# Optimization experiments

Hardware: AMD Instinct MI355X
Metric: run time of the kernel (lower is better)

The kernel has to match this reference:

```python
import jax, jax.numpy as jnp
import numpy as np

EMBED_DIM = 128
N_HEADS = 8
HEAD_DEPTH = EMBED_DIM // N_HEADS  # 16
CLIP = 10.0
B, N = 256, 1000


def setup_inputs() -> dict:
    key = jax.random.key(0)
    ks = jax.random.split(key, 10)
    D = EMBED_DIM
    return {
        "node_embeddings": jax.random.normal(ks[0], (B, N, D), jnp.float32),
        "graph_embedding": jax.random.normal(ks[1], (B, D), jnp.float32),
        "step_context": jax.random.normal(ks[2], (B, 1, D + 2), jnp.float32),
        "mask": jax.random.randint(ks[3], (B, 1, N), 0, 2).astype(bool),
        "Wk1": jax.random.normal(ks[4], (D, D), jnp.float32) / np.sqrt(D),
        "Wv": jax.random.normal(ks[5], (D, D), jnp.float32) / np.sqrt(D),
        "Wk2": jax.random.normal(ks[6], (D, D), jnp.float32) / np.sqrt(D),
        "Wq_fixed": jax.random.normal(ks[7], (D, D), jnp.float32) / np.sqrt(D),
        "Wout": jax.random.normal(ks[8], (D, D), jnp.float32) / np.sqrt(D),
        "Wq_step": jax.random.normal(ks[9], (D + 2, D), jnp.float32) / np.sqrt(D),
    }


def reference(node_embeddings, graph_embedding, step_context, mask,
              Wk1, Wv, Wk2, Wq_fixed, Wout, Wq_step):
    b, n, D = node_embeddings.shape
    H, dh = N_HEADS, HEAD_DEPTH
    neg_inf = jnp.float32(-1e9)

    # compute_static: precomputed projections of node/graph embeddings
    K1 = node_embeddings @ Wk1                      # [B,N,D]
    V = node_embeddings @ Wv                        # [B,N,D]
    K2 = node_embeddings @ Wk2                      # [B,N,D]
    Q_fixed = graph_embedding[:, None, :] @ Wq_fixed  # [B,1,D]

    # compute_dynamic: single-query masked MHA
    Q_step = step_context @ Wq_step                 # [B,1,D]
    Q1 = Q_fixed + Q_step                           # [B,1,D]
    q = Q1.reshape(b, 1, H, dh)
    k = K1.reshape(b, n, H, dh)
    v = V.reshape(b, n, H, dh)
    score = jnp.einsum('bqhd,bkhd->bhqk', q, k) / jnp.sqrt(jnp.float32(dh))
    score = jnp.where(mask[:, None, :, :], neg_inf, score)  # mask [B,1,N] -> [B,1,1,N]
    attn = jax.nn.softmax(score, axis=-1)           # [B,H,1,N]
    mha = jnp.einsum('bhqk,bkhd->bqhd', attn, v).reshape(b, 1, D)
    Q2 = mha @ Wout                                 # [B,1,D]

    # SHA: clipped single-head logits over all nodes
    logits = CLIP * jnp.tanh(
        jnp.einsum('bqd,bkd->bqk', Q2, K2) / jnp.sqrt(jnp.float32(D)))  # [B,1,N]
    logits = jnp.where(mask, neg_inf, logits)
    return logits[:, 0, :]                          # [B,N]
```

## Files before the change

### kernel.cpp

```cpp
#include <hip/hip_runtime.h>
#include <stdint.h>


#define DD 128
#define NH 8
#define DHD 16
#define NS 8
#define TILE 64
#define RP 132
#define SP 9
#define NMAX_PAD 1024

typedef short v8s __attribute__((ext_vector_type(8)));
typedef float v4f __attribute__((ext_vector_type(4)));

__device__ __forceinline__ unsigned short f2bf(float x) {
    unsigned u = __float_as_uint(x);
    u += 0x7fffu + ((u >> 16) & 1u);
    return (unsigned short)(u >> 16);
}

__device__ __forceinline__ bool detect_mask32(const void* maskp) {
    const uint32_t* mw = (const uint32_t*)maskp;
    bool m32 = true;
    #pragma unroll
    for (int i = 0; i < 16; ++i) m32 = m32 && (mw[i] <= 1u);
    return m32;
}

__global__ __launch_bounds__(128)
void k0_prep(const float* __restrict__ graph, const float* __restrict__ ctx,
             const float* __restrict__ Wk1, const float* __restrict__ Wqf,
             const float* __restrict__ Wqs, float* __restrict__ wq_ws)
{
    __shared__ float q1[DD];
    const int b = blockIdx.x, tid = threadIdx.x;
    const float* ge = graph + (size_t)b * DD;
    const float* sc = ctx + (size_t)b * (DD + 2);
    float acc = 0.f;
    #pragma unroll 4
    for (int k = 0; k < DD; ++k)     acc += ge[k] * Wqf[k * DD + tid];
    #pragma unroll 4
    for (int k = 0; k < DD + 2; ++k) acc += sc[k] * Wqs[k * DD + tid];
    q1[tid] = acc;
    __syncthreads();
    const float* wrow = Wk1 + (size_t)tid * DD;
    #pragma unroll
    for (int h = 0; h < NH; ++h) {
        float a = 0.f;
        #pragma unroll
        for (int j = 0; j < DHD; ++j) a += wrow[h * DHD + j] * q1[h * DHD + j];
        wq_ws[(size_t)b * NH * DD + h * DD + tid] = 0.25f * a;
    }
}

__global__ __launch_bounds__(512)
void kA_mfma(const float* __restrict__ node, const float* __restrict__ wq_ws,
             const void* __restrict__ maskp, float* __restrict__ spart_ws,
             float* __restrict__ mz_ws, int N)
{
    __shared__ __align__(16) unsigned short tA[2][8][64][16];
    __shared__ __align__(16) unsigned short Ph[2][16][72];
    __shared__ float wmax[16][9];
    __shared__ float zpart[16][9];
    __shared__ float mfin[16];

    const int b = blockIdx.y, j = blockIdx.x, tid = threadIdx.x;
    const int lane = tid & 63, w = tid >> 6;
    const int c = lane & 15, g = lane >> 4;
    const int rows = (N + NS - 1) / NS;
    const int n0 = j * rows;
    const int nend = min(n0 + rows, N);

    if (nend <= n0) {
        float* sp = spart_ws + ((size_t)b * NS + j) * NH * DD;
        for (int o = tid; o < NH * DD; o += 512) sp[o] = 0.f;
        if (tid < NH) {
            float* mzp = mz_ws + (((size_t)b * NS + j) * NH + tid) * 2;
            mzp[0] = -1e30f; mzp[1] = 0.f;
        }
        return;
    }

    const bool m32 = detect_mask32(maskp);
    const int32_t* mi = (const int32_t*)maskp + (size_t)b * N;
    const uint8_t* mb = (const uint8_t*)maskp + (size_t)b * N;
    const float* nodeB = node + (size_t)b * N * DD;

    v8s aw[4];
    #pragma unroll
    for (int kk = 0; kk < 4; ++kk) {
        v8s a;
        #pragma unroll
        for (int i = 0; i < 8; ++i) a[i] = 0;
        if (c < NH) {
            const float* wr = wq_ws + (size_t)b * NH * DD + (size_t)c * DD + kk * 32 + g * 8;
            #pragma unroll
            for (int i = 0; i < 8; ++i) a[i] = (short)f2bf(wr[i]);
        }
        aw[kk] = a;
    }

    {
        const int L = tid >> 3, c8 = tid & 7;
        #pragma unroll
        for (int t = 0; t < 2; ++t) {
            const int n = n0 + t * 64 + L;
            unsigned short tmp[16];
            if (n < nend) {
                const float4* src = (const float4*)(nodeB + (size_t)n * DD + c8 * 16);
                #pragma unroll
                for (int k = 0; k < 4; ++k) {
                    const float4 v = src[k];
                    tmp[4*k+0] = f2bf(v.x); tmp[4*k+1] = f2bf(v.y);
                    tmp[4*k+2] = f2bf(v.z); tmp[4*k+3] = f2bf(v.w);
                }
            } else {
                #pragma unroll
                for (int k = 0; k < 16; ++k) tmp[k] = 0;
            }
            *(v8s*)&tA[t][c8][L][0] = *(v8s*)&tmp[0];
            *(v8s*)&tA[t][c8][L][8] = *(v8s*)&tmp[8];
        }
    }
    __syncthreads();

    const int ts = w >> 2, rg = w & 3;
    const int nrow = n0 + ts * 64 + rg * 16 + c;
    v4f sc = {0.f, 0.f, 0.f, 0.f};
    #pragma unroll
    for (int kk = 0; kk < 4; ++kk) {
        const v8s bfrag = *(const v8s*)&tA[ts][kk * 2 + (g >> 1)][rg * 16 + c][(g & 1) * 8];
        sc = __builtin_amdgcn_mfma_f32_16x16x32_bf16(aw[kk], bfrag, sc, 0, 0, 0);
    }

    float s4[4];
    {
        const bool valid = nrow < nend;
        const bool msk = valid && (m32 ? (mi[nrow] != 0) : (mb[nrow] != 0));
        #pragma unroll
        for (int r = 0; r < 4; ++r)
            s4[r] = !valid ? -1e30f : (msk ? -1e9f : sc[r]);
    }

    {
        float mx[4];
        #pragma unroll
        for (int r = 0; r < 4; ++r) mx[r] = s4[r];
        #pragma unroll
        for (int d = 1; d < 16; d <<= 1) {
            #pragma unroll
            for (int r = 0; r < 4; ++r) mx[r] = fmaxf(mx[r], __shfl_xor(mx[r], d));
        }
        if (c == 0) {
            #pragma unroll
            for (int r = 0; r < 4; ++r) wmax[g * 4 + r][w] = mx[r];
        }
    }
    __syncthreads();
    if (w == 0 && lane < 16) {
        float m = wmax[lane][0];
        #pragma unroll
        for (int ww = 1; ww < 8; ++ww) m = fmaxf(m, wmax[lane][ww]);
        mfin[lane] = m;
    }
    __syncthreads();

    {
        float e4[4];
        #pragma unroll
        for (int r = 0; r < 4; ++r) e4[r] = __expf(s4[r] - mfin[g * 4 + r]);
        float zr[4];
        #pragma unroll
        for (int r = 0; r < 4; ++r) zr[r] = e4[r];
        #pragma unroll
        for (int d = 1; d < 16; d <<= 1) {
            #pragma unroll
            for (int r = 0; r < 4; ++r) zr[r] += __shfl_xor(zr[r], d);
        }
        if (c == 0) {
            #pragma unroll
            for (int r = 0; r < 4; ++r) zpart[g * 4 + r][w] = zr[r];
        }
        #pragma unroll
        for (int r = 0; r < 4; ++r)
            Ph[ts][g * 4 + r][rg * 16 + c] = f2bf(e4[r]);
    }
    __syncthreads();

    v4f c2 = {0.f, 0.f, 0.f, 0.f};
    #pragma unroll
    for (int s = 0; s < 4; ++s) {
        const int t2 = s >> 1, s1 = s & 1;
        const v8s pa = *(const v8s*)&Ph[t2][c][s1 * 32 + g * 8];
        v8s bb;
        #pragma unroll
        for (int i = 0; i < 8; ++i)
            bb[i] = (short)tA[t2][w][s1 * 32 + g * 8 + i][c];
        c2 = __builtin_amdgcn_mfma_f32_16x16x32_bf16(pa, bb, c2, 0, 0, 0);
    }

    if (g < 2) {
        float* sp = spart_ws + ((size_t)b * NS + j) * NH * DD;
        #pragma unroll
        for (int r = 0; r < 4; ++r)
            sp[(g * 4 + r) * DD + w * 16 + c] = c2[r];
    }
    if (w == 0 && lane < NH) {
        float z = 0.f;
        #pragma unroll
        for (int ww = 0; ww < 8; ++ww) z += zpart[lane][ww];
        float* mzp = mz_ws + (((size_t)b * NS + j) * NH + lane) * 2;
        mzp[0] = mfin[lane];
        mzp[1] = z;
    }
}

__global__ __launch_bounds__(128)
void kB_combine(const float* __restrict__ spart_ws, const float* __restrict__ mz_ws,
                const float* __restrict__ Wv, const float* __restrict__ Wout,
                const float* __restrict__ Wk2, float* __restrict__ w2_ws)
{
    __shared__ float m_l[NH * NS], z_l[NH * NS], wt[NH * NS];
    __shared__ float s_l[NH * DD];
    __shared__ float mha_l[DD];
    __shared__ float q2_l[DD];
    const int b = blockIdx.x, tid = threadIdx.x;

    if (tid < NH * NS) {
        const int h = tid >> 3, j = tid & 7;
        const float* mzp = mz_ws + (((size_t)b * NS + j) * NH + h) * 2;
        m_l[h * NS + j] = mzp[0];
        z_l[h * NS + j] = mzp[1];
    }
    __syncthreads();
    if (tid < NH) {
        const int h = tid;
        float M = -1e30f;
        #pragma unroll
        for (int j = 0; j < NS; ++j) M = fmaxf(M, m_l[h * NS + j]);
        float w[NS], Z = 0.f;
        #pragma unroll
        for (int j = 0; j < NS; ++j) {
            w[j] = __expf(m_l[h * NS + j] - M);
            Z += z_l[h * NS + j] * w[j];
        }
        const float rz = 1.f / Z;
        #pragma unroll
        for (int j = 0; j < NS; ++j) wt[h * NS + j] = w[j] * rz;
    }
    __syncthreads();
    const float* sp = spart_ws + (size_t)b * NS * NH * DD;
    for (int o = tid; o < NH * DD; o += 128) {
        const int h = o >> 7;
        float s = 0.f;
        #pragma unroll
        for (int j = 0; j < NS; ++j)
            s += sp[(size_t)j * NH * DD + o] * wt[h * NS + j];
        s_l[o] = s;
    }
    __syncthreads();
    {
        const int h = tid >> 4;
        float a = 0.f;
        for (int dp = 0; dp < DD; ++dp) a += s_l[h * DD + dp] * Wv[dp * DD + tid];
        mha_l[tid] = a;
    }
    __syncthreads();
    {
        float a = 0.f;
        for (int e = 0; e < DD; ++e) a += mha_l[e] * Wout[e * DD + tid];
        q2_l[tid] = a;
    }
    __syncthreads();
    {
        const float4* row = (const float4*)(Wk2 + (size_t)tid * DD);
        float a = 0.f;
        #pragma unroll
        for (int k = 0; k < 32; ++k) {
            const float4 w = row[k];
            a += w.x * q2_l[4*k] + w.y * q2_l[4*k+1] + w.z * q2_l[4*k+2] + w.w * q2_l[4*k+3];
        }
        w2_ws[(size_t)b * DD + tid] = a * 0.08838834764831845f;
    }
}

__global__ __launch_bounds__(256)
void k5_logits(const float* __restrict__ node, const float* __restrict__ w2_ws,
               const void* __restrict__ maskp, float* __restrict__ out, int N)
{
    const int b = blockIdx.y, j = blockIdx.x, tid = threadIdx.x;
    const int rows = (N + NS - 1) / NS;
    const int n0 = j * rows;
    const int nend = min(n0 + rows, N);
    const bool m32 = detect_mask32(maskp);
    const int32_t* mi = (const int32_t*)maskp + (size_t)b * N;
    const uint8_t* mb = (const uint8_t*)maskp + (size_t)b * N;
    const int sub = tid & 7, rr = tid >> 3;

    const float4* wv = (const float4*)(w2_ws + (size_t)b * DD + sub * 16);
    const float4 w0 = wv[0], w1 = wv[1], w2v = wv[2], w3 = wv[3];
    const float* nodeB = node + (size_t)b * N * DD;
    float* outB = out + (size_t)b * N;

    for (int n = n0 + rr; n < nend; n += 32) {
        const float4* nr = (const float4*)(nodeB + (size_t)n * DD + sub * 16);
        const float4 a0 = nr[0], a1 = nr[1], a2 = nr[2], a3 = nr[3];
        float p = a0.x*w0.x + a0.y*w0.y + a0.z*w0.z + a0.w*w0.w
                + a1.x*w1.x + a1.y*w1.y + a1.z*w1.z + a1.w*w1.w
                + a2.x*w2v.x + a2.y*w2v.y + a2.z*w2v.z + a2.w*w2v.w
                + a3.x*w3.x + a3.y*w3.y + a3.z*w3.z + a3.w*w3.w;
        p += __shfl_xor(p, 1);
        p += __shfl_xor(p, 2);
        p += __shfl_xor(p, 4);
        if (sub == 0) {
            const bool m = m32 ? (mi[n] != 0) : (mb[n] != 0);
            const float t = 1.f - 2.f / (__expf(2.f * p) + 1.f);
            outB[n] = m ? -1e9f : 10.f * t;
        }
    }
}

#define TPB 512
#define NMAX 1000
#define SPAD 9

__global__ __launch_bounds__(TPB)
void decoder_fallback(const float* __restrict__ node, const float* __restrict__ graph,
                      const float* __restrict__ ctx, const void* __restrict__ maskp,
                      const float* __restrict__ Wk1, const float* __restrict__ Wv,
                      const float* __restrict__ Wk2, const float* __restrict__ Wqf,
                      const float* __restrict__ Wout, const float* __restrict__ Wqs,
                      float* __restrict__ out, int N)
{
    __shared__ float node_tile[TILE * RP];
    __shared__ float scores[NMAX * SPAD];
    __shared__ float wq[NH * RP];
    __shared__ float s_lds[NH * RP];
    __shared__ float q1[DD];
    __shared__ float mha[DD];
    __shared__ float q2[DD];
    __shared__ float w2[DD];

    const int b = blockIdx.x, tid = threadIdx.x, lane = tid & 63, wave = tid >> 6;
    const bool mask32 = detect_mask32(maskp);
    const int32_t* mi = (const int32_t*)maskp + (size_t)b * N;
    const uint8_t* mb = (const uint8_t*)maskp + (size_t)b * N;
    const float* nodeB = node + (size_t)b * N * DD;

    if (tid < DD) {
        const float* ge = graph + (size_t)b * DD;
        const float* sc = ctx + (size_t)b * (DD + 2);
        float acc = 0.f;
        for (int k = 0; k < DD; ++k)     acc += ge[k] * Wqf[k * DD + tid];
        for (int k = 0; k < DD + 2; ++k) acc += sc[k] * Wqs[k * DD + tid];
        q1[tid] = acc;
    }
    __syncthreads();
    for (int idx = tid; idx < NH * DD; idx += TPB) {
        const int h = idx >> 7, dp = idx & (DD - 1);
        const float* wrow = Wk1 + dp * DD + h * DHD;
        float acc = 0.f;
        #pragma unroll
        for (int j = 0; j < DHD; ++j) acc += wrow[j] * q1[h * DHD + j];
        wq[h * RP + dp] = 0.25f * acc;
    }
    __syncthreads();
    const int ntiles = (N + TILE - 1) / TILE;
    const int n_local = tid >> 3, hA = tid & 7;
    for (int t = 0; t < ntiles; ++t) {
        const int n0 = t * TILE;
        #pragma unroll
        for (int cc = 0; cc < 4; ++cc) {
            const int idx = cc * (TPB * 4) + tid * 4;
            const int row = idx >> 7, col = idx & (DD - 1);
            if (n0 + row < N)
                *(float4*)&node_tile[row * RP + col] =
                    *(const float4*)(nodeB + (size_t)(n0 + row) * DD + col);
        }
        __syncthreads();
        if (n0 + n_local < N) {
            const float4* nr = (const float4*)&node_tile[n_local * RP];
            const float4* wr = (const float4*)&wq[hA * RP];
            float acc = 0.f;
            #pragma unroll
            for (int k = 0; k < DD / 4; ++k) {
                const float4 a = nr[k], wv = wr[k];
                acc += a.x * wv.x + a.y * wv.y + a.z * wv.z + a.w * wv.w;
            }
            scores[(n0 + n_local) * SPAD + hA] = acc;
        }
        __syncthreads();
    }
    {
        const int h = wave;
        float sm[16];
        #pragma unroll
        for (int k = 0; k < 16; ++k) {
            const int n = lane + 64 * k;
            float v = -1e9f;
            if (n < N) {
                const bool m = mask32 ? (mi[n] != 0) : (mb[n] != 0);
                v = m ? -1e9f : scores[n * SPAD + h];
            }
            sm[k] = v;
        }
        float mx = sm[0];
        #pragma unroll
        for (int k = 1; k < 16; ++k) mx = fmaxf(mx, sm[k]);
        #pragma unroll
        for (int d = 1; d < 64; d <<= 1) mx = fmaxf(mx, __shfl_xor(mx, d));
        float e[16];
        float sum = 0.f;
        #pragma unroll
        for (int k = 0; k < 16; ++k) {
            const int n = lane + 64 * k;
            e[k] = (n < N) ? __expf(sm[k] - mx) : 0.f;
            sum += e[k];
        }
        #pragma unroll
        for (int d = 1; d < 64; d <<= 1) sum += __shfl_xor(sum, d);
        const float rinv = 1.f / sum;
        #pragma unroll
        for (int k = 0; k < 16; ++k) {
            const int n = lane + 64 * k;
            if (n < N) scores[n * SPAD + h] = e[k] * rinv;
        }
    }
    __syncthreads();
    {
        const int h = wave;
        const float2* n2 = (const float2*)nodeB;
        float a0 = 0.f, a1 = 0.f;
        #pragma unroll 4
        for (int n = 0; n < N; ++n) {
            const float at = scores[n * SPAD + h];
            const float2 v = n2[(size_t)n * 64 + lane];
            a0 += at * v.x;
            a1 += at * v.y;
        }
        s_lds[h * RP + 2 * lane] = a0;
        s_lds[h * RP + 2 * lane + 1] = a1;
    }
    __syncthreads();
    if (tid < DD) {
        const int h = tid >> 4;
        float acc = 0.f;
        for (int dp = 0; dp < DD; ++dp) acc += s_lds[h * RP + dp] * Wv[dp * DD + tid];
        mha[tid] = acc;
    }
    __syncthreads();
    if (tid < DD) {
        float acc = 0.f;
        for (int e = 0; e < DD; ++e) acc += mha[e] * Wout[e * DD + tid];
        q2[tid] = acc;
    }
    __syncthreads();
    if (tid < DD) {
        const float4* row = (const float4*)(Wk2 + tid * DD);
        float acc = 0.f;
        #pragma unroll
        for (int k = 0; k < DD / 4; ++k) {
            const float4 wv = row[k];
            acc += wv.x * q2[4*k] + wv.y * q2[4*k+1] + wv.z * q2[4*k+2] + wv.w * q2[4*k+3];
        }
        w2[tid] = acc * 0.08838834764831845f;
    }
    __syncthreads();
    {
        const float wa = w2[2 * lane], wb = w2[2 * lane + 1];
        const float2* n2 = (const float2*)nodeB;
        float* outB = out + (size_t)b * N;
        for (int n = wave; n < N; n += NH) {
            const float2 v = n2[(size_t)n * 64 + lane];
            float p = v.x * wa + v.y * wb;
            #pragma unroll
            for (int d = 1; d < 64; d <<= 1) p += __shfl_xor(p, d);
            if (lane == 0) {
                const bool m = mask32 ? (mi[n] != 0) : (mb[n] != 0);
                const float t = 1.f - 2.f / (__expf(2.f * p) + 1.f);
                outB[n] = m ? -1e9f : 10.f * t;
            }
        }
    }
}

extern "C" void kernel_launch(void* const* d_in, const int* in_sizes, int n_in,
                              void* d_out, int out_size, void* d_ws, size_t ws_size,
                              hipStream_t stream) {
    (void)n_in; (void)out_size;
    const float* node  = (const float*)d_in[0];
    const float* graph = (const float*)d_in[1];
    const float* ctx   = (const float*)d_in[2];
    const void*  mask  = d_in[3];
    const float* Wk1   = (const float*)d_in[4];
    const float* Wv    = (const float*)d_in[5];
    const float* Wk2   = (const float*)d_in[6];
    const float* Wqf   = (const float*)d_in[7];
    const float* Wout  = (const float*)d_in[8];
    const float* Wqs   = (const float*)d_in[9];

    const int B = in_sizes[1] / DD;
    const int N = in_sizes[0] / (B * DD);

    const size_t off_wq    = 0;
    const size_t off_spart = off_wq + (size_t)B * NH * DD;
    const size_t off_mz    = off_spart + (size_t)B * NS * NH * DD;
    const size_t off_w2    = off_mz + (size_t)B * NS * NH * 2;
    const size_t need_f    = off_w2 + (size_t)B * DD;

    if (N <= NMAX_PAD && ws_size >= need_f * sizeof(float)) {
        float* ws       = (float*)d_ws;
        float* wq_ws    = ws + off_wq;
        float* spart_ws = ws + off_spart;
        float* mz_ws    = ws + off_mz;
        float* w2_ws    = ws + off_w2;

        k0_prep<<<B, 128, 0, stream>>>(graph, ctx, Wk1, Wqf, Wqs, wq_ws);
        kA_mfma<<<dim3(NS, B), 512, 0, stream>>>(node, wq_ws, mask, spart_ws, mz_ws, N);
        kB_combine<<<B, 128, 0, stream>>>(spart_ws, mz_ws, Wv, Wout, Wk2, w2_ws);
        k5_logits<<<dim3(NS, B), 256, 0, stream>>>(node, w2_ws, mask, (float*)d_out, N);
    } else {
        decoder_fallback<<<B, TPB, 0, stream>>>(node, graph, ctx, mask,
                                                Wk1, Wv, Wk2, Wqf, Wout, Wqs,
                                                (float*)d_out, N);
    }
}
```

Before: 97.45 us.

## Split attention pass into 16 smaller blocks, store bf16 partials, trim syncs

Doubles the number of node slices per batch (NS 8→16) and shrinks the attention kernel to 256 threads, each block handling one 64-row tile instead of two. Each thread now loads a full 32-float chunk of a node row up front, before the query weights are fetched, so the global loads are in flight earlier. The per-head max is now computed redundantly by every thread from the per-warp values, which drops one barrier and the mfin stage. The partial weighted sums are written in bf16 to halve workspace traffic. In exchange, the combine kernel must merge twice as many partials, and storing partials in bf16 adds rounding error.

```diff
diff --git a/kernel.cpp b/kernel.cpp
--- a/kernel.cpp
+++ b/kernel.cpp
@@ -5,10 +5,9 @@
 #define DD 128
 #define NH 8
 #define DHD 16
-#define NS 8
+#define NS 16
 #define TILE 64
 #define RP 132
-#define SP 9
 #define NMAX_PAD 1024
 
 typedef short v8s __attribute__((ext_vector_type(8)));
@@ -18,6 +17,9 @@
     unsigned u = __float_as_uint(x);
     u += 0x7fffu + ((u >> 16) & 1u);
     return (unsigned short)(u >> 16);
+}
+__device__ __forceinline__ float bf2f(unsigned short s) {
+    return __uint_as_float((unsigned)s << 16);
 }
 
 __device__ __forceinline__ bool detect_mask32(const void* maskp) {
@@ -54,16 +56,15 @@
     }
 }
 
-__global__ __launch_bounds__(512)
+__global__ __launch_bounds__(256)
 void kA_mfma(const float* __restrict__ node, const float* __restrict__ wq_ws,
-             const void* __restrict__ maskp, float* __restrict__ spart_ws,
+             const void* __restrict__ maskp, unsigned short* __restrict__ spart_ws,
              float* __restrict__ mz_ws, int N)
 {
-    __shared__ __align__(16) unsigned short tA[2][8][64][16];
-    __shared__ __align__(16) unsigned short Ph[2][16][72];
-    __shared__ float wmax[16][9];
-    __shared__ float zpart[16][9];
-    __shared__ float mfin[16];
+    __shared__ __align__(16) unsigned short tA[8][TILE][16];
+    __shared__ __align__(16) unsigned short Ph[16][72];
+    __shared__ float wmax[16][5];
+    __shared__ float zpart[16][5];
 
     const int b = blockIdx.y, j = blockIdx.x, tid = threadIdx.x;
     const int lane = tid & 63, w = tid >> 6;
@@ -73,8 +74,8 @@
     const int nend = min(n0 + rows, N);
 
     if (nend <= n0) {
-        float* sp = spart_ws + ((size_t)b * NS + j) * NH * DD;
-        for (int o = tid; o < NH * DD; o += 512) sp[o] = 0.f;
+        unsigned short* sp = spart_ws + ((size_t)b * NS + j) * NH * DD;
+        for (int o = tid; o < NH * DD; o += 256) sp[o] = 0;
         if (tid < NH) {
             float* mzp = mz_ws + (((size_t)b * NS + j) * NH + tid) * 2;
             mzp[0] = -1e30f; mzp[1] = 0.f;
@@ -82,10 +83,37 @@
         return;
     }
 
-    const bool m32 = detect_mask32(maskp);
-    const int32_t* mi = (const int32_t*)maskp + (size_t)b * N;
-    const uint8_t* mb = (const uint8_t*)maskp + (size_t)b * N;
     const float* nodeB = node + (size_t)b * N * DD;
+
+    const int L = tid >> 2, q = tid & 3;
+    {
+        const int n = n0 + L;
+        const bool valid = n < nend;
+        const int srcrow = valid ? n : (nend - 1);
+        const float4* src = (const float4*)(nodeB + (size_t)srcrow * DD + q * 32);
+        float4 f[8];
+        #pragma unroll
+        for (int k = 0; k < 8; ++k) f[k] = src[k];
+
+        unsigned short tmp[32];
+        #pragma unroll
+        for (int k = 0; k < 8; ++k) {
+            tmp[4*k+0] = valid ? f2bf(f[k].x) : (unsigned short)0;
+            tmp[4*k+1] = valid ? f2bf(f[k].y) : (unsigned short)0;
+            tmp[4*k+2] = valid ? f2bf(f[k].z) : (unsigned short)0;
+            tmp[4*k+3] = valid ? f2bf(f[k].w) : (unsigned short)0;
+        }
+        v8s t0, t1, t2, t3;
+        #pragma unroll
+        for (int i = 0; i < 8; ++i) {
+            t0[i] = (short)tmp[i];      t1[i] = (short)tmp[8 + i];
+            t2[i] = (short)tmp[16 + i]; t3[i] = (short)tmp[24 + i];
+        }
+        *(v8s*)&tA[2*q][L][0]   = t0;
+        *(v8s*)&tA[2*q][L][8]   = t1;
+        *(v8s*)&tA[2*q+1][L][0] = t2;
+        *(v8s*)&tA[2*q+1][L][8] = t3;
+    }
 
     v8s aw[4];
     #pragma unroll
@@ -101,36 +129,17 @@
         aw[kk] = a;
     }
 
-    {
-        const int L = tid >> 3, c8 = tid & 7;
-        #pragma unroll
-        for (int t = 0; t < 2; ++t) {
-            const int n = n0 + t * 64 + L;
-            unsigned short tmp[16];
-            if (n < nend) {
-                const float4* src = (const float4*)(nodeB + (size_t)n * DD + c8 * 16);
-                #pragma unroll
-                for (int k = 0; k < 4; ++k) {
-                    const float4 v = src[k];
-                    tmp[4*k+0] = f2bf(v.x); tmp[4*k+1] = f2bf(v.y);
-                    tmp[4*k+2] = f2bf(v.z); tmp[4*k+3] = f2bf(v.w);
-                }
-            } else {
-                #pragma unroll
-                for (int k = 0; k < 16; ++k) tmp[k] = 0;
-            }
-            *(v8s*)&tA[t][c8][L][0] = *(v8s*)&tmp[0];
-            *(v8s*)&tA[t][c8][L][8] = *(v8s*)&tmp[8];
-        }
-    }
-    __syncthreads();
-
-    const int ts = w >> 2, rg = w & 3;
-    const int nrow = n0 + ts * 64 + rg * 16 + c;
+    const bool m32 = detect_mask32(maskp);
+    const int32_t* mi = (const int32_t*)maskp + (size_t)b * N;
+    const uint8_t* mb = (const uint8_t*)maskp + (size_t)b * N;
+
+    __syncthreads();
+
+    const int nrow = n0 + w * 16 + c;
     v4f sc = {0.f, 0.f, 0.f, 0.f};
     #pragma unroll
     for (int kk = 0; kk < 4; ++kk) {
-        const v8s bfrag = *(const v8s*)&tA[ts][kk * 2 + (g >> 1)][rg * 16 + c][(g & 1) * 8];
+        const v8s bfrag = *(const v8s*)&tA[2*kk + (g >> 1)][w * 16 + c][(g & 1) * 8];
         sc = __builtin_amdgcn_mfma_f32_16x16x32_bf16(aw[kk], bfrag, sc, 0, 0, 0);
     }
 
@@ -158,18 +167,16 @@
         }
     }
     __syncthreads();
-    if (w == 0 && lane < 16) {
-        float m = wmax[lane][0];
-        #pragma unroll
-        for (int ww = 1; ww < 8; ++ww) m = fmaxf(m, wmax[lane][ww]);
-        mfin[lane] = m;
-    }
-    __syncthreads();
 
     {
         float e4[4];
         #pragma unroll
-        for (int r = 0; r < 4; ++r) e4[r] = __expf(s4[r] - mfin[g * 4 + r]);
+        for (int r = 0; r < 4; ++r) {
+            const int h = g * 4 + r;
+            const float m = fmaxf(fmaxf(wmax[h][0], wmax[h][1]),
+                                  fmaxf(wmax[h][2], wmax[h][3]));
+            e4[r] = __expf(s4[r] - m);
+        }
         float zr[4];
         #pragma unroll
         for (int r = 0; r < 4; ++r) zr[r] = e4[r];
@@ -184,40 +191,45 @@
         }
         #pragma unroll
         for (int r = 0; r < 4; ++r)
-            Ph[ts][g * 4 + r][rg * 16 + c] = f2bf(e4[r]);
-    }
-    __syncthreads();
-
-    v4f c2 = {0.f, 0.f, 0.f, 0.f};
+            Ph[g * 4 + r][w * 16 + c] = f2bf(e4[r]);
+    }
+    __syncthreads();
+
+    v4f c0 = {0.f, 0.f, 0.f, 0.f}, c1 = {0.f, 0.f, 0.f, 0.f};
     #pragma unroll
-    for (int s = 0; s < 4; ++s) {
-        const int t2 = s >> 1, s1 = s & 1;
-        const v8s pa = *(const v8s*)&Ph[t2][c][s1 * 32 + g * 8];
-        v8s bb;
-        #pragma unroll
-        for (int i = 0; i < 8; ++i)
-            bb[i] = (short)tA[t2][w][s1 * 32 + g * 8 + i][c];
-        c2 = __builtin_amdgcn_mfma_f32_16x16x32_bf16(pa, bb, c2, 0, 0, 0);
+    for (int sl = 0; sl < 2; ++sl) {
+        const v8s pa = *(const v8s*)&Ph[c][sl * 32 + g * 8];
+        v8s bb0, bb1;
+        #pragma unroll
+        for (int i = 0; i < 8; ++i) {
+            const int kr = sl * 32 + g * 8 + i;
+            bb0[i] = (short)tA[2*w][kr][c];
+            bb1[i] = (short)tA[2*w+1][kr][c];
+        }
+        c0 = __builtin_amdgcn_mfma_f32_16x16x32_bf16(pa, bb0, c0, 0, 0, 0);
+        c1 = __builtin_amdgcn_mfma_f32_16x16x32_bf16(pa, bb1, c1, 0, 0, 0);
     }
 
     if (g < 2) {
-        float* sp = spart_ws + ((size_t)b * NS + j) * NH * DD;
-        #pragma unroll
-        for (int r = 0; r < 4; ++r)
-            sp[(g * 4 + r) * DD + w * 16 + c] = c2[r];
-    }
-    if (w == 0 && lane < NH) {
-        float z = 0.f;
-        #pragma unroll
-        for (int ww = 0; ww < 8; ++ww) z += zpart[lane][ww];
-        float* mzp = mz_ws + (((size_t)b * NS + j) * NH + lane) * 2;
-        mzp[0] = mfin[lane];
+        unsigned short* sp = spart_ws + ((size_t)b * NS + j) * NH * DD;
+        #pragma unroll
+        for (int r = 0; r < 4; ++r) {
+            sp[(g * 4 + r) * DD + (2*w)     * 16 + c] = f2bf(c0[r]);
+            sp[(g * 4 + r) * DD + (2*w + 1) * 16 + c] = f2bf(c1[r]);
+        }
+    }
+    if (tid < NH) {
+        const float z = zpart[tid][0] + zpart[tid][1] + zpart[tid][2] + zpart[tid][3];
+        const float m = fmaxf(fmaxf(wmax[tid][0], wmax[tid][1]),
+                              fmaxf(wmax[tid][2], wmax[tid][3]));
+        float* mzp = mz_ws + (((size_t)b * NS + j) * NH + tid) * 2;
+        mzp[0] = m;
         mzp[1] = z;
     }
 }
 
 __global__ __launch_bounds__(128)
-void kB_combine(const float* __restrict__ spart_ws, const float* __restrict__ mz_ws,
+void kB_combine(const unsigned short* __restrict__ spart_ws, const float* __restrict__ mz_ws,
                 const float* __restrict__ Wv, const float* __restrict__ Wout,
                 const float* __restrict__ Wk2, float* __restrict__ w2_ws)
 {
@@ -227,8 +239,8 @@
     __shared__ float q2_l[DD];
     const int b = blockIdx.x, tid = threadIdx.x;
 
-    if (tid < NH * NS) {
-        const int h = tid >> 3, j = tid & 7;
+    {
+        const int h = tid >> 4, j = tid & 15;
         const float* mzp = mz_ws + (((size_t)b * NS + j) * NH + h) * 2;
         m_l[h * NS + j] = mzp[0];
         z_l[h * NS + j] = mzp[1];
@@ -239,24 +251,25 @@
         float M = -1e30f;
         #pragma unroll
         for (int j = 0; j < NS; ++j) M = fmaxf(M, m_l[h * NS + j]);
-        float w[NS], Z = 0.f;
+        float Z = 0.f;
+        float wv[NS];
         #pragma unroll
         for (int j = 0; j < NS; ++j) {
-            w[j] = __expf(m_l[h * NS + j] - M);
-            Z += z_l[h * NS + j] * w[j];
+            wv[j] = __expf(m_l[h * NS + j] - M);
+            Z += z_l[h * NS + j] * wv[j];
         }
         const float rz = 1.f / Z;
         #pragma unroll
-        for (int j = 0; j < NS; ++j) wt[h * NS + j] = w[j] * rz;
-    }
-    __syncthreads();
-    const float* sp = spart_ws + (size_t)b * NS * NH * DD;
+        for (int j = 0; j < NS; ++j) wt[h * NS + j] = wv[j] * rz;
+    }
+    __syncthreads();
+    const unsigned short* sp = spart_ws + (size_t)b * NS * NH * DD;
     for (int o = tid; o < NH * DD; o += 128) {
         const int h = o >> 7;
         float s = 0.f;
         #pragma unroll
         for (int j = 0; j < NS; ++j)
-            s += sp[(size_t)j * NH * DD + o] * wt[h * NS + j];
+            s += bf2f(sp[(size_t)j * NH * DD + o]) * wt[h * NS + j];
         s_l[o] = s;
     }
     __syncthreads();
@@ -503,21 +516,21 @@
     const int B = in_sizes[1] / DD;
     const int N = in_sizes[0] / (B * DD);
 
-    const size_t off_wq    = 0;
-    const size_t off_spart = off_wq + (size_t)B * NH * DD;
-    const size_t off_mz    = off_spart + (size_t)B * NS * NH * DD;
-    const size_t off_w2    = off_mz + (size_t)B * NS * NH * 2;
-    const size_t need_f    = off_w2 + (size_t)B * DD;
-
-    if (N <= NMAX_PAD && ws_size >= need_f * sizeof(float)) {
-        float* ws       = (float*)d_ws;
-        float* wq_ws    = ws + off_wq;
-        float* spart_ws = ws + off_spart;
-        float* mz_ws    = ws + off_mz;
-        float* w2_ws    = ws + off_w2;
+    const size_t wq_bytes    = (size_t)B * NH * DD * 4;
+    const size_t spart_bytes = (size_t)B * NS * NH * DD * 2;
+    const size_t mz_bytes    = (size_t)B * NS * NH * 2 * 4;
+    const size_t w2_bytes    = (size_t)B * DD * 4;
+    const size_t need_bytes  = wq_bytes + spart_bytes + mz_bytes + w2_bytes;
+
+    if (N <= NMAX_PAD && ws_size >= need_bytes) {
+        char* ws = (char*)d_ws;
+        float*          wq_ws    = (float*)ws;
+        unsigned short* spart_ws = (unsigned short*)(ws + wq_bytes);
+        float*          mz_ws    = (float*)(ws + wq_bytes + spart_bytes);
+        float*          w2_ws    = (float*)(ws + wq_bytes + spart_bytes + mz_bytes);
 
         k0_prep<<<B, 128, 0, stream>>>(graph, ctx, Wk1, Wqf, Wqs, wq_ws);
-        kA_mfma<<<dim3(NS, B), 512, 0, stream>>>(node, wq_ws, mask, spart_ws, mz_ws, N);
+        kA_mfma<<<dim3(NS, B), 256, 0, stream>>>(node, wq_ws, mask, spart_ws, mz_ws, N);
         kB_combine<<<B, 128, 0, stream>>>(spart_ws, mz_ws, Wv, Wout, Wk2, w2_ws);
         k5_logits<<<dim3(NS, B), 256, 0, stream>>>(node, w2_ws, mask, (float*)d_out, N);
     } else {
```

Result: slower. 103.1 us (+5.8%).
